# Kernel tuning notes

Hardware: AMD Instinct MI355X
Metric: run time of the kernel (lower is better)

## Reference

```python
import jax, jax.numpy as jnp
import numpy as np

BINS = 100
NORMALIZE = False
SIGMA = 1.0
B, N = 128, 512
EDGE_P = 0.02  # edge probability -> avg degree ~10


def _make_adj(key):
    u = jax.random.uniform(key, (B, N, N))
    a = (u < EDGE_P).astype(jnp.float32)
    up = jnp.triu(a, 1)
    return up + jnp.swapaxes(up, -1, -2)  # symmetric, zero diagonal


def setup_inputs() -> dict:
    key = jax.random.key(0)
    k1, k2 = jax.random.split(key)
    return {"adj_1": _make_adj(k1), "adj_2": _make_adj(k2)}


def _clustering_hist(adj):
    # adj: [B, N, N] binary symmetric, zero diag
    deg = adj.sum(-1)                                   # [B, N]
    a2 = jnp.matmul(adj, adj)                           # [B, N, N]
    tri2 = jnp.einsum('bij,bji->bi', a2, adj)           # diag(A^3) = 2 * triangles
    denom = deg * (deg - 1.0)
    # nx.clustering: c_i = 2*T_i / (k_i*(k_i-1)) = diag(A^3)_i / (k_i*(k_i-1)); 0 if k_i < 2
    c = jnp.where(denom > 0, tri2 / jnp.maximum(denom, 1.0), 0.0)  # [B, N] in [0,1]
    # histogram over [0,1] with BINS bins; value 1.0 falls in last bin (torch.histogram semantics)
    idx = jnp.clip((c * BINS).astype(jnp.int32), 0, BINS - 1)
    hist = jax.vmap(lambda ix: jnp.zeros((BINS,), jnp.float32).at[ix].add(1.0))(idx)
    if NORMALIZE:
        hist = hist * (BINS / N)  # density: count / (n_samples * bin_width)
    return hist  # [B, BINS]


def _rbf_mmd(x, y, sigma):
    # biased MMD^2 estimate with RBF kernel
    def kmat(a, b):
        sq = (a * a).sum(-1)[:, None] + (b * b).sum(-1)[None, :] - 2.0 * (a @ b.T)
        return jnp.exp(-jnp.maximum(sq, 0.0) / (2.0 * sigma * sigma))
    return kmat(x, x).mean() + kmat(y, y).mean() - 2.0 * kmat(x, y).mean()


def reference(adj_1, adj_2):
    h1 = _clustering_hist(adj_1)
    h2 = _clustering_hist(adj_2)
    return _rbf_mmd(h1, h2, SIGMA)
```

## Files before the change

kernel.cpp:

```cpp
#include <hip/hip_runtime.h>
#include <stdint.h>

#define BATCH 128
#define NN 512
#define BINS 100
#define WORDS 8
#define WPAD 9
#define ECAP 6144

__device__ __forceinline__ unsigned long long spread4(unsigned long long x) {
    x = (x | (x << 24)) & 0x000000ff000000ffull;
    x = (x | (x << 12)) & 0x000f000f000f000full;
    x = (x | (x <<  6)) & 0x0303030303030303ull;
    x = (x | (x <<  3)) & 0x1111111111111111ull;
    return x;
}

__global__ __launch_bounds__(1024) void k_cluster_hist(
    const float* __restrict__ adj1, const float* __restrict__ adj2,
    float* __restrict__ hist ,
    unsigned int* __restrict__ mmd_cnt)
{
    __shared__ unsigned long long bits[NN][WPAD];
    __shared__ unsigned int edges[ECAP];
    __shared__ int tri2[NN];
    __shared__ int histI[BINS];
    __shared__ int ecnt;

    const int gb = blockIdx.x;
    const float* __restrict__ gp =
        (gb < BATCH ? adj1 : adj2) + (size_t)(gb & (BATCH - 1)) * NN * NN;

    const int tid  = threadIdx.x;
    const int lane = tid & 63;
    const int wave = tid >> 6;

    if (tid < BINS) histI[tid] = 0;
    if (tid < NN)   tri2[tid]  = 0;
    if (tid == 0)   ecnt = 0;
    if (gb == 0 && tid == 0) *mmd_cnt = 0;

    const int rot = (gb * 73) & (NN - 1);
    for (int k = 0; k < 32; ++k) {
        const int r  = (wave + (k << 4) + rot) & (NN - 1);
        const int br = r >> 6;
        const int nb = 8 - br;
        const int c0 = br << 6;
        const int rr = r & 63;
        const int Lmin = (rr < 3) ? 0 : ((rr + 1) >> 2);
        float4 v = make_float4(0.f, 0.f, 0.f, 0.f);
        if (lane < 16 * nb && (lane >= 16 || lane >= Lmin))
            v = *(const float4*)(gp + (size_t)r * NN + c0 + 4 * lane);
        unsigned long long b0 = __ballot(v.x != 0.0f);
        unsigned long long b1 = __ballot(v.y != 0.0f);
        unsigned long long b2 = __ballot(v.z != 0.0f);
        unsigned long long b3 = __ballot(v.w != 0.0f);
        if (lane < nb) {
            const int sh = 16 * lane;
            unsigned long long w =
                (spread4((b0 >> sh) & 0xFFFFull) << 0) |
                (spread4((b1 >> sh) & 0xFFFFull) << 1) |
                (spread4((b2 >> sh) & 0xFFFFull) << 2) |
                (spread4((b3 >> sh) & 0xFFFFull) << 3);
            bits[r][br + lane] = w;
        }
    }
    __syncthreads();

    for (int p = wave; p < 36; p += 16) {
        int bi, bj;
        if (p < 28) {
            bi = 1;
            while (bi * (bi + 1) / 2 <= p) ++bi;
            bj = p - bi * (bi - 1) / 2;
        } else {
            bi = p - 28; bj = bi;
        }
        unsigned long long x = bits[(bj << 6) + lane][bi];
        unsigned long long t = x;
        const unsigned long long M[6] = {
            0x5555555555555555ull, 0x3333333333333333ull,
            0x0f0f0f0f0f0f0f0full, 0x00ff00ff00ff00ffull,
            0x0000ffff0000ffffull, 0x00000000ffffffffull };
        #pragma unroll
        for (int s = 0; s < 6; ++s) {
            const int k = 1 << s;
            unsigned long long y = __shfl_xor((long long)t, k, 64);
            if ((lane & k) == 0) t = (t &  M[s]) | ((y &  M[s]) << k);
            else                 t = (t & ~M[s]) | ((y & ~M[s]) >> k);
        }
        if (p < 28) bits[(bi << 6) + lane][bj] = t;
        else        bits[(bi << 6) + lane][bi] = x | t;
    }
    __syncthreads();

    for (int p = tid; p < NN * WORDS; p += 1024) {
        int r = p >> 3;
        int m = p & 7;
        unsigned long long w = bits[r][m];
        int base = m << 6;
        int sh = r - base + 1;
        unsigned long long wm =
            (sh <= 0) ? w : (sh >= 64 ? 0ull : (w & (~0ull << sh)));
        int cnt = __popcll(wm);

        int x = cnt;
        #pragma unroll
        for (int off = 1; off < 64; off <<= 1) {
            int y = __shfl_up(x, off, 64);
            if (lane >= off) x += y;
        }
        int excl = x - cnt;
        int bs = 0;
        if (lane == 63) bs = atomicAdd(&ecnt, x);
        bs = __shfl(bs, 63, 64);

        int idx = bs + excl;
        while (wm) {
            int L = __builtin_ctzll(wm);
            wm &= wm - 1;
            int j = base + L;
            if (idx < ECAP) edges[idx] = ((unsigned)r << 10) | (unsigned)j;
            ++idx;
        }
    }
    __syncthreads();

    const int ne = ecnt < ECAP ? ecnt : ECAP;
    for (int e = tid; e < ne; e += 1024) {
        unsigned ed = edges[e];
        int i = ed >> 10;
        int j = ed & 1023;
        int acc = 0;
        #pragma unroll
        for (int w = 0; w < WORDS; ++w)
            acc += __popcll(bits[i][w] & bits[j][w]);
        atomicAdd(&tri2[i], acc);
        atomicAdd(&tri2[j], acc);
    }
    __syncthreads();

    if (tid < NN) {
        int deg = 0;
        #pragma unroll
        for (int w = 0; w < WORDS; ++w) deg += __popcll(bits[tid][w]);
        float t2    = (float)tri2[tid];
        float degf  = (float)deg;
        float denom = degf * (degf - 1.0f);
        float c = denom > 0.0f ? t2 / denom : 0.0f;
        int idx = (int)(c * 100.0f);
        idx = idx < 0 ? 0 : (idx > BINS - 1 ? BINS - 1 : idx);
        atomicAdd(&histI[idx], 1);
    }
    __syncthreads();

    if (tid < BINS) hist[(size_t)gb * BINS + tid] = (float)histI[tid];
}

__global__ __launch_bounds__(256) void k_mmd(
    const float* __restrict__ hist, float* __restrict__ partials,
    unsigned int* __restrict__ cnt, float* __restrict__ out)
{
    int p = blockIdx.x * 256 + threadIdx.x;
    int t   = p >> 14;
    int rem = p & 16383;
    int i = rem >> 7;
    int j = rem & 127;
    const float4* x4;
    const float4* y4;
    float w;
    if (t == 0)      { x4 = (const float4*)(hist + (size_t)i * BINS);           y4 = (const float4*)(hist + (size_t)j * BINS);           w =  1.0f; }
    else if (t == 1) { x4 = (const float4*)(hist + (size_t)(BATCH + i) * BINS); y4 = (const float4*)(hist + (size_t)(BATCH + j) * BINS); w =  1.0f; }
    else             { x4 = (const float4*)(hist + (size_t)i * BINS);           y4 = (const float4*)(hist + (size_t)(BATCH + j) * BINS); w = -2.0f; }
    float sq = 0.0f;
    #pragma unroll
    for (int k = 0; k < BINS / 4; ++k) {
        float4 a = x4[k];
        float4 b = y4[k];
        float d0 = a.x - b.x, d1 = a.y - b.y, d2 = a.z - b.z, d3 = a.w - b.w;
        sq += d0 * d0 + d1 * d1 + d2 * d2 + d3 * d3;
    }
    float local = w * expf(-0.5f * sq);

    __shared__ float red[256];
    __shared__ bool amLast;
    red[threadIdx.x] = local;
    __syncthreads();
    for (int s = 128; s >= 1; s >>= 1) {
        if (threadIdx.x < s) red[threadIdx.x] += red[threadIdx.x + s];
        __syncthreads();
    }
    if (threadIdx.x == 0) {
        partials[blockIdx.x] = red[0];
        __threadfence();
        amLast = (atomicAdd(cnt, 1u) == 191u);
    }
    __syncthreads();
    if (amLast) {
        __threadfence();
        if (threadIdx.x < 64) {
            float v = 0.0f;
            for (int q = threadIdx.x; q < 192; q += 64) v += partials[q];
            #pragma unroll
            for (int off = 32; off >= 1; off >>= 1) v += __shfl_xor(v, off, 64);
            if (threadIdx.x == 0) out[0] = v * (1.0f / (float)(BATCH * BATCH));
        }
    }
}

extern "C" void kernel_launch(void* const* d_in, const int* in_sizes, int n_in,
                              void* d_out, int out_size, void* d_ws, size_t ws_size,
                              hipStream_t stream) {
    const float* a1 = (const float*)d_in[0];
    const float* a2 = (const float*)d_in[1];
    float* out = (float*)d_out;

    const size_t hist_bytes = (size_t)2 * BATCH * BINS * 4;
    float* hist            = (float*)d_ws;
    float* partials        = (float*)((char*)d_ws + hist_bytes);
    unsigned int* mmd_cnt  = (unsigned int*)((char*)d_ws + hist_bytes + 1024);

    hipLaunchKernelGGL(k_cluster_hist, dim3(2 * BATCH), dim3(1024), 0, stream,
                       a1, a2, hist, mmd_cnt);
    hipLaunchKernelGGL(k_mmd, dim3(192), dim3(256), 0, stream,
                       hist, partials, mmd_cnt, out);
}
```

Before: 261.2 us.

## Load top half fully and bottom-right quadrant, mirror cross block by transpose

```diff
diff --git a/kernel.cpp b/kernel.cpp
--- a/kernel.cpp
+++ b/kernel.cpp
@@ -40,44 +40,60 @@
     if (tid == 0)   ecnt = 0;
     if (gb == 0 && tid == 0) *mmd_cnt = 0;
 
-    const int rot = (gb * 73) & (NN - 1);
-    for (int k = 0; k < 32; ++k) {
-        const int r  = (wave + (k << 4) + rot) & (NN - 1);
-        const int br = r >> 6;
-        const int nb = 8 - br;
-        const int c0 = br << 6;
-        const int rr = r & 63;
-        const int Lmin = (rr < 3) ? 0 : ((rr + 1) >> 2);
-        float4 v = make_float4(0.f, 0.f, 0.f, 0.f);
-        if (lane < 16 * nb && (lane >= 16 || lane >= Lmin))
-            v = *(const float4*)(gp + (size_t)r * NN + c0 + 4 * lane);
-        unsigned long long b0 = __ballot(v.x != 0.0f);
-        unsigned long long b1 = __ballot(v.y != 0.0f);
-        unsigned long long b2 = __ballot(v.z != 0.0f);
-        unsigned long long b3 = __ballot(v.w != 0.0f);
-        if (lane < nb) {
+    for (int k = 0; k < 16; ++k) {
+        const int r = wave + (k << 4);
+        const float* rp = gp + (size_t)r * NN;
+        float4 v0 = *(const float4*)(rp + 4 * lane);
+        float4 v1 = *(const float4*)(rp + 256 + 4 * lane);
+        unsigned long long a0 = __ballot(v0.x != 0.0f);
+        unsigned long long a1 = __ballot(v0.y != 0.0f);
+        unsigned long long a2 = __ballot(v0.z != 0.0f);
+        unsigned long long a3 = __ballot(v0.w != 0.0f);
+        unsigned long long c0 = __ballot(v1.x != 0.0f);
+        unsigned long long c1 = __ballot(v1.y != 0.0f);
+        unsigned long long c2 = __ballot(v1.z != 0.0f);
+        unsigned long long c3 = __ballot(v1.w != 0.0f);
+        if (lane < 8) {
+            const int d  = lane;
+            const int sh = 16 * (d & 3);
+            unsigned long long w;
+            if (d < 4)
+                w = (spread4((a0 >> sh) & 0xFFFFull) << 0) |
+                    (spread4((a1 >> sh) & 0xFFFFull) << 1) |
+                    (spread4((a2 >> sh) & 0xFFFFull) << 2) |
+                    (spread4((a3 >> sh) & 0xFFFFull) << 3);
+            else
+                w = (spread4((c0 >> sh) & 0xFFFFull) << 0) |
+                    (spread4((c1 >> sh) & 0xFFFFull) << 1) |
+                    (spread4((c2 >> sh) & 0xFFFFull) << 2) |
+                    (spread4((c3 >> sh) & 0xFFFFull) << 3);
+            bits[r][d] = w;
+        }
+    }
+    for (int k = 16; k < 32; ++k) {
+        const int r = wave + (k << 4);
+        const float* rp = gp + (size_t)r * NN;
+        float4 v1 = *(const float4*)(rp + 256 + 4 * lane);
+        unsigned long long c0 = __ballot(v1.x != 0.0f);
+        unsigned long long c1 = __ballot(v1.y != 0.0f);
+        unsigned long long c2 = __ballot(v1.z != 0.0f);
+        unsigned long long c3 = __ballot(v1.w != 0.0f);
+        if (lane < 4) {
             const int sh = 16 * lane;
             unsigned long long w =
-                (spread4((b0 >> sh) & 0xFFFFull) << 0) |
-                (spread4((b1 >> sh) & 0xFFFFull) << 1) |
-                (spread4((b2 >> sh) & 0xFFFFull) << 2) |
-                (spread4((b3 >> sh) & 0xFFFFull) << 3);
-            bits[r][br + lane] = w;
-        }
-    }
-    __syncthreads();
-
-    for (int p = wave; p < 36; p += 16) {
-        int bi, bj;
-        if (p < 28) {
-            bi = 1;
-            while (bi * (bi + 1) / 2 <= p) ++bi;
-            bj = p - bi * (bi - 1) / 2;
-        } else {
-            bi = p - 28; bj = bi;
-        }
-        unsigned long long x = bits[(bj << 6) + lane][bi];
-        unsigned long long t = x;
+                (spread4((c0 >> sh) & 0xFFFFull) << 0) |
+                (spread4((c1 >> sh) & 0xFFFFull) << 1) |
+                (spread4((c2 >> sh) & 0xFFFFull) << 2) |
+                (spread4((c3 >> sh) & 0xFFFFull) << 3);
+            bits[r][4 + lane] = w;
+        }
+    }
+    __syncthreads();
+
+    {
+        const int bi = 4 + (wave >> 2);
+        const int bj = wave & 3;
+        unsigned long long t = bits[(bj << 6) + lane][bi];
         const unsigned long long M[6] = {
             0x5555555555555555ull, 0x3333333333333333ull,
             0x0f0f0f0f0f0f0f0full, 0x00ff00ff00ff00ffull,
@@ -89,8 +105,7 @@
             if ((lane & k) == 0) t = (t &  M[s]) | ((y &  M[s]) << k);
             else                 t = (t & ~M[s]) | ((y & ~M[s]) >> k);
         }
-        if (p < 28) bits[(bi << 6) + lane][bj] = t;
-        else        bits[(bi << 6) + lane][bi] = x | t;
+        bits[(bi << 6) + lane][bj] = t;
     }
     __syncthreads();
 
```

New measurement: 276.4 us. +5.8%, slower.
